# Kernel tuning notes

Measured on AMD Instinct MI355X. Metric: run time of the kernel, lower is better.

Reference implementation:

```python
import jax, jax.numpy as jnp
import numpy as np
from jax import lax

L, B, S, D, H = 2, 8, 2048, 1024, 1024
LOG_H0 = float(np.log(0.5))  # h0 = g(0) = 0.5


def _log_g(x):
    # log of g(x) = x + 0.5 if x >= 0 else sigmoid(x)
    return jnp.where(x >= 0, jnp.log(jnp.where(x >= 0, x + 0.5, 1.0)), -jax.nn.softplus(-x))


def _mingru_layer(x, Wz, bz, Wh, bh):
    # x: (B,S,D) -> (B,S,H) via log-space heinsen associative scan
    k = jnp.einsum('bsd,hd->bsh', x, Wz) + bz          # gate pre-activation
    log_z = -jax.nn.softplus(-k)                        # log sigmoid(k)
    log_coeffs = -jax.nn.softplus(k)                    # log (1 - sigmoid(k))
    pre_h = jnp.einsum('bsd,hd->bsh', x, Wh) + bh
    log_values = log_z + _log_g(pre_h)                  # log(z * h_tilde)
    Bq = x.shape[0]
    # prepend initial state: coeff 0 (log 1), value log(h0)
    log_coeffs = jnp.pad(log_coeffs, ((0, 0), (1, 0), (0, 0)))
    log_values = jnp.concatenate(
        [jnp.full((Bq, 1, log_values.shape[-1]), LOG_H0, dtype=log_values.dtype), log_values], axis=1)
    a_star = jnp.cumsum(log_coeffs, axis=1)
    log_h = a_star + lax.cumlogsumexp(log_values - a_star, axis=1)
    return jnp.exp(log_h)[:, 1:]


def setup_inputs() -> dict:
    key = jax.random.key(0)
    ks = jax.random.split(key, 5)
    stdv = 1.0 / np.sqrt(D)
    u = lambda k, shp: jax.random.uniform(k, shp, jnp.float32, -stdv, stdv)
    return {
        'x': jax.random.normal(ks[0], (B, S, D), jnp.float32),
        'Wz': u(ks[1], (L, H, D)),
        'bz': u(ks[2], (L, H)),
        'Wh': u(ks[3], (L, H, D)),
        'bh': u(ks[4], (L, H)),
    }


def reference(x, Wz, bz, Wh, bh):
    h = x
    for l in range(Wz.shape[0]):
        h = _mingru_layer(h, Wz[l], bz[l], Wh[l], bh[l])
    return h  # (B,S,H), last layer outputs
```

## Files before the change

kernel.cpp:

```cpp
#include <hip/hip_runtime.h>
#include <hip/hip_bf16.h>


#define L_ 2
#define B_ 8
#define S_ 2048
#define D_ 1024
#define H_ 1024
#define M_ (B_*S_)
#define NC 32
#define CL (S_/NC)

typedef __bf16    bf16x8 __attribute__((ext_vector_type(8)));
typedef float     f32x4  __attribute__((ext_vector_type(4)));
typedef _Float16  h2     __attribute__((ext_vector_type(2)));
typedef _Float16  h4     __attribute__((ext_vector_type(4)));

__device__ __forceinline__ ushort f2bf(float f) {
    union { __hip_bfloat16 h; ushort u; } c;
    c.h = __float2bfloat16(f);
    return c.u;
}

__device__ __forceinline__ void async16(const void* g, void* l) {
    __builtin_amdgcn_global_load_lds(
        (const __attribute__((address_space(1))) unsigned int*)g,
        (__attribute__((address_space(3))) unsigned int*)l, 16, 0, 0);
}

__global__ __launch_bounds__(256) void cast_f32_bf16(const float* __restrict__ in,
                                                     ushort* __restrict__ out, int n4) {
    int i = blockIdx.x * 256 + threadIdx.x;
    if (i >= n4) return;
    float4 v = ((const float4*)in)[i];
    ushort4 o;
    o.x = f2bf(v.x); o.y = f2bf(v.y); o.z = f2bf(v.z); o.w = f2bf(v.w);
    ((ushort4*)out)[i] = o;
}

#define SWZ(R, c) (((R) << 6) + ((((c) ^ ((R) & 7))) << 3))

__global__ __launch_bounds__(256) void gemm_fused(const ushort* __restrict__ A,
                                                  const ushort* __restrict__ Wz,
                                                  const ushort* __restrict__ Wh,
                                                  const float* __restrict__ bz,
                                                  const float* __restrict__ bh,
                                                  h2* __restrict__ cv,
                                                  float* __restrict__ Ac,
                                                  float* __restrict__ Bc)
{
    __shared__ __align__(16) ushort sm[16384];
    ushort* As = sm;
    ushort* Zs = sm + 8192;
    ushort* Hs = sm + 12288;

    const int t    = threadIdx.x;
    const int lane = t & 63;
    const int wave = t >> 6;
    const int xcd = (int)blockIdx.x & 7;
    const int k8  = (int)blockIdx.x >> 3;
    const int nblk = k8 & 15;
    const int mblk = ((k8 >> 4) << 3) + xcd;
    const int m0 = mblk * 128;
    const int n0 = nblk * 64;
    const int wm = (wave >> 1) * 64;
    const int wn = (wave & 1) * 32;

    const int srow   = lane >> 3;
    const int scol_g = (((lane & 7) ^ srow) << 3);

    f32x4 accz[4][2] = {};
    f32x4 acch[4][2] = {};
    const int lrow = lane & 15;
    const int lcq  = lane >> 4;

    for (int kb = 0; kb < D_; kb += 64) {
        __syncthreads();
        #pragma unroll
        for (int i = 0; i < 4; ++i) {
            int r = i*32 + wave*8;
            async16(&A[(size_t)(m0 + r + srow)*D_ + kb + scol_g], &As[r*64]);
        }
        #pragma unroll
        for (int i = 0; i < 2; ++i) {
            int r = i*32 + wave*8;
            async16(&Wz[(size_t)(n0 + r + srow)*D_ + kb + scol_g], &Zs[r*64]);
            async16(&Wh[(size_t)(n0 + r + srow)*D_ + kb + scol_g], &Hs[r*64]);
        }
        __syncthreads();
        #pragma unroll
        for (int kk = 0; kk < 64; kk += 32) {
            const int cq = (kk >> 3) + lcq;
            bf16x8 af[4];
            #pragma unroll
            for (int mt = 0; mt < 4; ++mt) {
                int R = wm + mt*16 + lrow;
                uint4 u = *(const uint4*)&As[SWZ(R, cq)];
                af[mt] = __builtin_bit_cast(bf16x8, u);
            }
            #pragma unroll
            for (int nt = 0; nt < 2; ++nt) {
                int R = wn + nt*16 + lrow;
                uint4 uz = *(const uint4*)&Zs[SWZ(R, cq)];
                uint4 uh = *(const uint4*)&Hs[SWZ(R, cq)];
                bf16x8 zb = __builtin_bit_cast(bf16x8, uz);
                bf16x8 hb = __builtin_bit_cast(bf16x8, uh);
                #pragma unroll
                for (int mt = 0; mt < 4; ++mt) {
                    accz[mt][nt] = __builtin_amdgcn_mfma_f32_16x16x32_bf16(af[mt], zb, accz[mt][nt], 0, 0, 0);
                    acch[mt][nt] = __builtin_amdgcn_mfma_f32_16x16x32_bf16(af[mt], hb, acch[mt][nt], 0, 0, 0);
                }
            }
        }
    }

    __syncthreads();
    float2* seg = (float2*)sm;

    const int colq = lane & 15;
    const int rowq = (lane >> 4) * 4;
    #pragma unroll
    for (int nt = 0; nt < 2; ++nt) {
        const int n = n0 + wn + nt*16 + colq;
        const float bzv = bz[n];
        const float bhv = bh[n];
        #pragma unroll
        for (int mt = 0; mt < 4; ++mt) {
            float a = 1.f, bb = 0.f;
            #pragma unroll
            for (int r = 0; r < 4; ++r) {
                const int m = m0 + wm + mt*16 + rowq + r;
                float k = accz[mt][nt][r] + bzv;
                float p = acch[mt][nt][r] + bhv;
                float e   = __expf(-fabsf(k));
                float inv = 1.0f / (1.0f + e);
                float z   = (k >= 0.f) ? inv     : e * inv;
                float c   = (k >= 0.f) ? e * inv : inv;
                float g;
                if (p >= 0.f) g = p + 0.5f;
                else { float eg = __expf(p); g = eg / (1.0f + eg); }
                float v = z * g;
                h2 hv; hv[0] = (_Float16)c; hv[1] = (_Float16)v;
                cv[(size_t)m * H_ + n] = hv;
                bb = fmaf(c, bb, v);
                a *= c;
            }
            const int sidx = (wm >> 2) + mt*4 + (rowq >> 2);
            seg[sidx*65 + wn + nt*16 + colq] = make_float2(a, bb);
        }
    }
    __syncthreads();
    if (t < 128) {
        const int col  = t & 63;
        const int half = t >> 6;
        float a = 1.f, bb = 0.f;
        #pragma unroll
        for (int s = 0; s < 16; ++s) {
            float2 e = seg[(half*16 + s)*65 + col];
            bb = fmaf(e.x, bb, e.y);
            a *= e.x;
        }
        const int b     = m0 >> 11;
        const int chunk = ((m0 >> 6) & (NC - 1)) + half;
        const int q = (b*NC + chunk)*H_ + n0 + col;
        Ac[q] = a; Bc[q] = bb;
    }
}

__global__ __launch_bounds__(256) void scan_chunk_combine(const float* __restrict__ Ac,
                                                          const float* __restrict__ Bc,
                                                          float* __restrict__ hin)
{
    int q = blockIdx.x * 256 + threadIdx.x;
    int h = q & (H_-1);
    int b = q >> 10;
    float hcur = 0.5f;
    #pragma unroll
    for (int c = 0; c < NC; ++c) {
        int idx = (b*NC + c)*H_ + h;
        hin[idx] = hcur;
        hcur = fmaf(Ac[idx], hcur, Bc[idx]);
    }
}

__global__ __launch_bounds__(256) void scan_emit(const h2* __restrict__ cv,
                                                 const float* __restrict__ hin,
                                                 float* __restrict__ outf,
                                                 ushort* __restrict__ outb,
                                                 const int write_bf16)
{
    int q = blockIdx.x * 256 + threadIdx.x;
    int hp = (q & 511) * 2;
    int c = (q >> 9) & (NC-1);
    int b = q >> 14;
    size_t base = (size_t)(b*S_ + c*CL) * H_ + hp;
    int qh = (b*NC + c)*H_ + hp;
    float h0 = hin[qh], h1 = hin[qh + 1];
    if (write_bf16) {
        #pragma unroll 4
        for (int tt = 0; tt < CL; ++tt) {
            h4 e = *(const h4*)&cv[base + (size_t)tt * H_];
            h0 = fmaf((float)e[0], h0, (float)e[1]);
            h1 = fmaf((float)e[2], h1, (float)e[3]);
            ushort2 o; o.x = f2bf(h0); o.y = f2bf(h1);
            *(ushort2*)&outb[base + (size_t)tt * H_] = o;
        }
    } else {
        #pragma unroll 4
        for (int tt = 0; tt < CL; ++tt) {
            h4 e = *(const h4*)&cv[base + (size_t)tt * H_];
            h0 = fmaf((float)e[0], h0, (float)e[1]);
            h1 = fmaf((float)e[2], h1, (float)e[3]);
            *(float2*)&outf[base + (size_t)tt * H_] = make_float2(h0, h1);
        }
    }
}

extern "C" void kernel_launch(void* const* d_in, const int* in_sizes, int n_in,
                              void* d_out, int out_size, void* d_ws, size_t ws_size,
                              hipStream_t stream)
{
    const float* x  = (const float*)d_in[0];
    const float* Wz = (const float*)d_in[1];
    const float* bz = (const float*)d_in[2];
    const float* Wh = (const float*)d_in[3];
    const float* bh = (const float*)d_in[4];
    float* out = (float*)d_out;

    ushort* xb  = (ushort*)d_ws;
    ushort* wzb = xb  + (size_t)M_*D_;
    ushort* whb = wzb + (size_t)L_*H_*D_;
    h2*     cv  = (h2*)(whb + (size_t)L_*H_*D_);
    float*  Ac  = (float*)(cv + (size_t)M_*H_);
    float*  Bc  = Ac + B_*NC*H_;
    float*  hin = Bc + B_*NC*H_;

    cast_f32_bf16<<<(M_*D_/4)/256, 256, 0, stream>>>(x, xb, M_*D_/4);
    cast_f32_bf16<<<(L_*H_*D_/4)/256, 256, 0, stream>>>(Wz, wzb, L_*H_*D_/4);
    cast_f32_bf16<<<(L_*H_*D_/4)/256, 256, 0, stream>>>(Wh, whb, L_*H_*D_/4);

    const int gemm_grid = (M_/128) * (H_/64);
    for (int l = 0; l < L_; ++l) {
        gemm_fused<<<gemm_grid, 256, 0, stream>>>(xb,
                                                  wzb + (size_t)l*H_*D_,
                                                  whb + (size_t)l*H_*D_,
                                                  bz + l*H_, bh + l*H_,
                                                  cv, Ac, Bc);
        scan_chunk_combine<<<(B_*H_)/256, 256, 0, stream>>>(Ac, Bc, hin);
        scan_emit<<<(B_*NC*H_/2)/256, 256, 0, stream>>>(cv, hin, out, xb, (l == 0) ? 1 : 0);
    }
}
```

Baseline: 340.9 us.

## Double-buffer GEMM loads, fuse casts, merge chunk combine into emit, repack cv layout

The GEMM's K loop is double-buffered in 64KB of dynamic LDS, with async loads for the next stage issued before computing the current one and waited on with vmcnt. The three cast kernels become one launch. The chunk-combine kernel is removed: each scan_emit thread recomputes its chunk's carry-in serially from Ac/Bc. The cv intermediate is repacked so four timesteps for one column are stored contiguously as one 16-byte write and read. This trades fewer launches and better load overlap for redundant carry work, scalar output stores with one column per thread, and lower GEMM occupancy from the larger LDS use.

```diff
diff --git a/kernel.cpp b/kernel.cpp
--- a/kernel.cpp
+++ b/kernel.cpp
@@ -14,7 +14,7 @@
 typedef __bf16    bf16x8 __attribute__((ext_vector_type(8)));
 typedef float     f32x4  __attribute__((ext_vector_type(4)));
 typedef _Float16  h2     __attribute__((ext_vector_type(2)));
-typedef _Float16  h4     __attribute__((ext_vector_type(4)));
+typedef _Float16  h8     __attribute__((ext_vector_type(8)));
 
 __device__ __forceinline__ ushort f2bf(float f) {
     union { __hip_bfloat16 h; ushort u; } c;
@@ -28,17 +28,35 @@
         (__attribute__((address_space(3))) unsigned int*)l, 16, 0, 0);
 }
 
-__global__ __launch_bounds__(256) void cast_f32_bf16(const float* __restrict__ in,
-                                                     ushort* __restrict__ out, int n4) {
+__global__ __launch_bounds__(256) void cast_all(const float* __restrict__ x,
+                                                const float* __restrict__ Wz,
+                                                const float* __restrict__ Wh,
+                                                ushort* __restrict__ xb,
+                                                ushort* __restrict__ wzb,
+                                                ushort* __restrict__ whb) {
+    const int nw = L_*H_*D_/4;
     int i = blockIdx.x * 256 + threadIdx.x;
-    if (i >= n4) return;
-    float4 v = ((const float4*)in)[i];
-    ushort4 o;
-    o.x = f2bf(v.x); o.y = f2bf(v.y); o.z = f2bf(v.z); o.w = f2bf(v.w);
-    ((ushort4*)out)[i] = o;
+    {
+        float4 v = ((const float4*)x)[i];
+        ushort4 o;
+        o.x = f2bf(v.x); o.y = f2bf(v.y); o.z = f2bf(v.z); o.w = f2bf(v.w);
+        ((ushort4*)xb)[i] = o;
+    }
+    if (i < nw) {
+        float4 v = ((const float4*)Wz)[i];
+        ushort4 o;
+        o.x = f2bf(v.x); o.y = f2bf(v.y); o.z = f2bf(v.z); o.w = f2bf(v.w);
+        ((ushort4*)wzb)[i] = o;
+        float4 w = ((const float4*)Wh)[i];
+        ushort4 p;
+        p.x = f2bf(w.x); p.y = f2bf(w.y); p.z = f2bf(w.z); p.w = f2bf(w.w);
+        ((ushort4*)whb)[i] = p;
+    }
 }
 
 #define SWZ(R, c) (((R) << 6) + ((((c) ^ ((R) & 7))) << 3))
+#define MFMA16 __builtin_amdgcn_mfma_f32_16x16x32_bf16
+#define FENCE() asm volatile("" ::: "memory")
 
 __global__ __launch_bounds__(256) void gemm_fused(const ushort* __restrict__ A,
                                                   const ushort* __restrict__ Wz,
@@ -49,10 +67,7 @@
                                                   float* __restrict__ Ac,
                                                   float* __restrict__ Bc)
 {
-    __shared__ __align__(16) ushort sm[16384];
-    ushort* As = sm;
-    ushort* Zs = sm + 8192;
-    ushort* Hs = sm + 12288;
+    extern __shared__ __align__(16) ushort sm[];
 
     const int t    = threadIdx.x;
     const int lane = t & 63;
@@ -74,20 +89,35 @@
     const int lrow = lane & 15;
     const int lcq  = lane >> 4;
 
-    for (int kb = 0; kb < D_; kb += 64) {
-        __syncthreads();
-        #pragma unroll
-        for (int i = 0; i < 4; ++i) {
-            int r = i*32 + wave*8;
-            async16(&A[(size_t)(m0 + r + srow)*D_ + kb + scol_g], &As[r*64]);
-        }
-        #pragma unroll
-        for (int i = 0; i < 2; ++i) {
-            int r = i*32 + wave*8;
-            async16(&Wz[(size_t)(n0 + r + srow)*D_ + kb + scol_g], &Zs[r*64]);
-            async16(&Wh[(size_t)(n0 + r + srow)*D_ + kb + scol_g], &Hs[r*64]);
-        }
-        __syncthreads();
+    #define STAGE(kb, bo)                                                      \
+        do {                                                                   \
+            _Pragma("unroll")                                                  \
+            for (int i_ = 0; i_ < 4; ++i_) {                  \
+                int r_ = i_*32 + wave*8;                                       \
+                async16(&A[(size_t)(m0 + r_ + srow)*D_ + (kb) + scol_g],       \
+                        &sm[(bo) + r_*64]);                                    \
+            }                                                                  \
+            _Pragma("unroll")                                                  \
+            for (int i_ = 0; i_ < 2; ++i_) {              \
+                int r_ = i_*32 + wave*8;                                       \
+                async16(&Wz[(size_t)(n0 + r_ + srow)*D_ + (kb) + scol_g],      \
+                        &sm[(bo) + 8192 + r_*64]);                             \
+                async16(&Wh[(size_t)(n0 + r_ + srow)*D_ + (kb) + scol_g],      \
+                        &sm[(bo) + 12288 + r_*64]);                            \
+            }                                                                  \
+        } while (0)
+
+    STAGE(0, 0);
+
+    #pragma unroll 2
+    for (int tt = 0; tt < 16; ++tt) {
+        const int cur = (tt & 1) << 14;
+        const int nxt = cur ^ 16384;
+        const int kbn = (tt < 15 ? tt + 1 : 15) << 6;
+        STAGE(kbn, nxt);
+        asm volatile("s_waitcnt vmcnt(8)" ::: "memory");
+        __builtin_amdgcn_s_barrier();
+        FENCE();
         #pragma unroll
         for (int kk = 0; kk < 64; kk += 32) {
             const int cq = (kk >> 3) + lcq;
@@ -95,30 +125,33 @@
             #pragma unroll
             for (int mt = 0; mt < 4; ++mt) {
                 int R = wm + mt*16 + lrow;
-                uint4 u = *(const uint4*)&As[SWZ(R, cq)];
+                uint4 u = *(const uint4*)&sm[cur + SWZ(R, cq)];
                 af[mt] = __builtin_bit_cast(bf16x8, u);
             }
             #pragma unroll
             for (int nt = 0; nt < 2; ++nt) {
                 int R = wn + nt*16 + lrow;
-                uint4 uz = *(const uint4*)&Zs[SWZ(R, cq)];
-                uint4 uh = *(const uint4*)&Hs[SWZ(R, cq)];
+                uint4 uz = *(const uint4*)&sm[cur + 8192  + SWZ(R, cq)];
+                uint4 uh = *(const uint4*)&sm[cur + 12288 + SWZ(R, cq)];
                 bf16x8 zb = __builtin_bit_cast(bf16x8, uz);
                 bf16x8 hb = __builtin_bit_cast(bf16x8, uh);
                 #pragma unroll
                 for (int mt = 0; mt < 4; ++mt) {
-                    accz[mt][nt] = __builtin_amdgcn_mfma_f32_16x16x32_bf16(af[mt], zb, accz[mt][nt], 0, 0, 0);
-                    acch[mt][nt] = __builtin_amdgcn_mfma_f32_16x16x32_bf16(af[mt], hb, acch[mt][nt], 0, 0, 0);
+                    accz[mt][nt] = MFMA16(af[mt], zb, accz[mt][nt], 0, 0, 0);
+                    acch[mt][nt] = MFMA16(af[mt], hb, acch[mt][nt], 0, 0, 0);
                 }
             }
         }
-    }
-
+        FENCE();
+        __builtin_amdgcn_s_barrier();
+    }
+
+    asm volatile("s_waitcnt vmcnt(0)" ::: "memory");
     __syncthreads();
+
     float2* seg = (float2*)sm;
-
     const int colq = lane & 15;
-    const int rowq = (lane >> 4) * 4;
+    const int rowq = (lane >> 4) << 2;
     #pragma unroll
     for (int nt = 0; nt < 2; ++nt) {
         const int n = n0 + wn + nt*16 + colq;
@@ -127,24 +160,26 @@
         #pragma unroll
         for (int mt = 0; mt < 4; ++mt) {
             float a = 1.f, bb = 0.f;
+            h8 pk;
             #pragma unroll
             for (int r = 0; r < 4; ++r) {
-                const int m = m0 + wm + mt*16 + rowq + r;
-                float k = accz[mt][nt][r] + bzv;
-                float p = acch[mt][nt][r] + bhv;
-                float e   = __expf(-fabsf(k));
+                float kx = accz[mt][nt][r] + bzv;
+                float p  = acch[mt][nt][r] + bhv;
+                float e   = __expf(-fabsf(kx));
                 float inv = 1.0f / (1.0f + e);
-                float z   = (k >= 0.f) ? inv     : e * inv;
-                float c   = (k >= 0.f) ? e * inv : inv;
+                float z   = (kx >= 0.f) ? inv     : e * inv;
+                float c   = (kx >= 0.f) ? e * inv : inv;
                 float g;
                 if (p >= 0.f) g = p + 0.5f;
                 else { float eg = __expf(p); g = eg / (1.0f + eg); }
                 float v = z * g;
-                h2 hv; hv[0] = (_Float16)c; hv[1] = (_Float16)v;
-                cv[(size_t)m * H_ + n] = hv;
+                pk[2*r]     = (_Float16)c;
+                pk[2*r + 1] = (_Float16)v;
                 bb = fmaf(c, bb, v);
                 a *= c;
             }
+            const int mb4 = (m0 + wm + mt*16 + rowq) >> 2;
+            *(h8*)&cv[((size_t)mb4 * H_ + n) * 4] = pk;
             const int sidx = (wm >> 2) + mt*4 + (rowq >> 2);
             seg[sidx*65 + wn + nt*16 + colq] = make_float2(a, bb);
         }
@@ -156,62 +191,54 @@
         float a = 1.f, bb = 0.f;
         #pragma unroll
         for (int s = 0; s < 16; ++s) {
-            float2 e = seg[(half*16 + s)*65 + col];
-            bb = fmaf(e.x, bb, e.y);
-            a *= e.x;
+            float2 e2 = seg[(half*16 + s)*65 + col];
+            bb = fmaf(e2.x, bb, e2.y);
+            a *= e2.x;
         }
         const int b     = m0 >> 11;
         const int chunk = ((m0 >> 6) & (NC - 1)) + half;
         const int q = (b*NC + chunk)*H_ + n0 + col;
         Ac[q] = a; Bc[q] = bb;
     }
-}
-
-__global__ __launch_bounds__(256) void scan_chunk_combine(const float* __restrict__ Ac,
-                                                          const float* __restrict__ Bc,
-                                                          float* __restrict__ hin)
-{
-    int q = blockIdx.x * 256 + threadIdx.x;
-    int h = q & (H_-1);
-    int b = q >> 10;
-    float hcur = 0.5f;
-    #pragma unroll
-    for (int c = 0; c < NC; ++c) {
-        int idx = (b*NC + c)*H_ + h;
-        hin[idx] = hcur;
-        hcur = fmaf(Ac[idx], hcur, Bc[idx]);
-    }
+    #undef STAGE
 }
 
 __global__ __launch_bounds__(256) void scan_emit(const h2* __restrict__ cv,
-                                                 const float* __restrict__ hin,
+                                                 const float* __restrict__ Ac,
+                                                 const float* __restrict__ Bc,
                                                  float* __restrict__ outf,
                                                  ushort* __restrict__ outb,
                                                  const int write_bf16)
 {
     int q = blockIdx.x * 256 + threadIdx.x;
-    int hp = (q & 511) * 2;
-    int c = (q >> 9) & (NC-1);
-    int b = q >> 14;
-    size_t base = (size_t)(b*S_ + c*CL) * H_ + hp;
-    int qh = (b*NC + c)*H_ + hp;
-    float h0 = hin[qh], h1 = hin[qh + 1];
+    int h = q & (H_-1);
+    int c = (q >> 10) & (NC-1);
+    int b = q >> 15;
+    float hc = 0.5f;
+    for (int cp = 0; cp < c; ++cp) {
+        int idx = (b*NC + cp)*H_ + h;
+        hc = fmaf(Ac[idx], hc, Bc[idx]);
+    }
+    const int mb = b*S_ + c*CL;
     if (write_bf16) {
         #pragma unroll 4
-        for (int tt = 0; tt < CL; ++tt) {
-            h4 e = *(const h4*)&cv[base + (size_t)tt * H_];
-            h0 = fmaf((float)e[0], h0, (float)e[1]);
-            h1 = fmaf((float)e[2], h1, (float)e[3]);
-            ushort2 o; o.x = f2bf(h0); o.y = f2bf(h1);
-            *(ushort2*)&outb[base + (size_t)tt * H_] = o;
+        for (int j = 0; j < 16; ++j) {
+            h8 e = *(const h8*)&cv[(((size_t)(mb >> 2) + j)*H_ + h) * 4];
+            #pragma unroll
+            for (int u = 0; u < 4; ++u) {
+                hc = fmaf((float)e[2*u], hc, (float)e[2*u + 1]);
+                outb[(size_t)(mb + 4*j + u)*H_ + h] = f2bf(hc);
+            }
         }
     } else {
         #pragma unroll 4
-        for (int tt = 0; tt < CL; ++tt) {
-            h4 e = *(const h4*)&cv[base + (size_t)tt * H_];
-            h0 = fmaf((float)e[0], h0, (float)e[1]);
-            h1 = fmaf((float)e[2], h1, (float)e[3]);
-            *(float2*)&outf[base + (size_t)tt * H_] = make_float2(h0, h1);
+        for (int j = 0; j < 16; ++j) {
+            h8 e = *(const h8*)&cv[(((size_t)(mb >> 2) + j)*H_ + h) * 4];
+            #pragma unroll
+            for (int u = 0; u < 4; ++u) {
+                hc = fmaf((float)e[2*u], hc, (float)e[2*u + 1]);
+                outf[(size_t)(mb + 4*j + u)*H_ + h] = hc;
+            }
         }
     }
 }
@@ -227,26 +254,30 @@
     const float* bh = (const float*)d_in[4];
     float* out = (float*)d_out;
 
+    static bool attr_set = false;
+    if (!attr_set) {
+        (void)hipFuncSetAttribute(reinterpret_cast<const void*>(gemm_fused),
+                                  hipFuncAttributeMaxDynamicSharedMemorySize, 65536);
+        attr_set = true;
+    }
+
     ushort* xb  = (ushort*)d_ws;
     ushort* wzb = xb  + (size_t)M_*D_;
     ushort* whb = wzb + (size_t)L_*H_*D_;
     h2*     cv  = (h2*)(whb + (size_t)L_*H_*D_);
     float*  Ac  = (float*)(cv + (size_t)M_*H_);
     float*  Bc  = Ac + B_*NC*H_;
-    float*  hin = Bc + B_*NC*H_;
-
-    cast_f32_bf16<<<(M_*D_/4)/256, 256, 0, stream>>>(x, xb, M_*D_/4);
-    cast_f32_bf16<<<(L_*H_*D_/4)/256, 256, 0, stream>>>(Wz, wzb, L_*H_*D_/4);
-    cast_f32_bf16<<<(L_*H_*D_/4)/256, 256, 0, stream>>>(Wh, whb, L_*H_*D_/4);
+
+    cast_all<<<(M_*D_/4)/256, 256, 0, stream>>>(x, Wz, Wh, xb, wzb, whb);
 
     const int gemm_grid = (M_/128) * (H_/64);
     for (int l = 0; l < L_; ++l) {
-        gemm_fused<<<gemm_grid, 256, 0, stream>>>(xb,
-                                                  wzb + (size_t)l*H_*D_,
-                                                  whb + (size_t)l*H_*D_,
-                                                  bz + l*H_, bh + l*H_,
-                                                  cv, Ac, Bc);
-        scan_chunk_combine<<<(B_*H_)/256, 256, 0, stream>>>(Ac, Bc, hin);
-        scan_emit<<<(B_*NC*H_/2)/256, 256, 0, stream>>>(cv, hin, out, xb, (l == 0) ? 1 : 0);
-    }
-}
+        gemm_fused<<<gemm_grid, 256, 65536, stream>>>(xb,
+                                                      wzb + (size_t)l*H_*D_,
+                                                      whb + (size_t)l*H_*D_,
+                                                      bz + l*H_, bh + l*H_,
+                                                      cv, Ac, Bc);
+        scan_emit<<<(B_*NC*H_)/256, 256, 0, stream>>>(cv, Ac, Bc, out, xb,
+                                                      (l == 0) ? 1 : 0);
+    }
+}
```

Measured after the change: 343.6 us. No clear change (+0.8%).
